# Kernel optimization log

Hardware: AMD Instinct MI355X
Metric: run time of the kernel (lower is better)

Reference implementation:

```python
import jax, jax.numpy as jnp
import numpy as np

N_NODES = 100000
N_EDGES = 1600000
N_PAIRS = 200000
IN_CH = 128
HID_CH = 128


def _graph_conv(x, src, dst, edge_weight, w_rel, b_rel, w_root, num_nodes):
    # PyG GraphConv with aggr='mean':
    # out = lin_rel(mean_{j in N(i)}(x_j * w_ij)) + lin_root(x_i)
    msg = x[src] * edge_weight[:, None]                       # [E, C] gather
    agg = jax.ops.segment_sum(msg, dst, num_segments=num_nodes)  # [N, C]
    cnt = jax.ops.segment_sum(jnp.ones((src.shape[0],), x.dtype), dst,
                              num_segments=num_nodes)          # in-degree
    agg = agg / jnp.maximum(cnt, 1.0)[:, None]                 # mean aggr
    return agg @ w_rel + b_rel + x @ w_root


def setup_inputs() -> dict:
    key = jax.random.key(0)
    ks = jax.random.split(key, 10)
    x = jax.random.normal(ks[0], (N_NODES, IN_CH), dtype=jnp.float32)
    edge_index = jax.random.randint(ks[1], (2, N_EDGES), 0, N_NODES, dtype=jnp.int32)
    edge_weight = jax.random.uniform(ks[2], (N_EDGES,), dtype=jnp.float32)
    edge_label_index = jax.random.randint(ks[3], (2, N_PAIRS), 0, N_NODES, dtype=jnp.int32)
    s1 = 1.0 / np.sqrt(IN_CH)
    s2 = 1.0 / np.sqrt(HID_CH)
    w1_rel = jax.random.uniform(ks[4], (IN_CH, HID_CH), jnp.float32, -s1, s1)
    b1_rel = jnp.zeros((HID_CH,), jnp.float32)
    w1_root = jax.random.uniform(ks[5], (IN_CH, HID_CH), jnp.float32, -s1, s1)
    w2_rel = jax.random.uniform(ks[6], (HID_CH, HID_CH), jnp.float32, -s2, s2)
    b2_rel = jnp.zeros((HID_CH,), jnp.float32)
    w2_root = jax.random.uniform(ks[7], (HID_CH, HID_CH), jnp.float32, -s2, s2)
    return {"x": x, "edge_index": edge_index, "edge_weight": edge_weight,
            "edge_label_index": edge_label_index,
            "w1_rel": w1_rel, "b1_rel": b1_rel, "w1_root": w1_root,
            "w2_rel": w2_rel, "b2_rel": b2_rel, "w2_root": w2_root}


def reference(x, edge_index, edge_weight, edge_label_index,
              w1_rel, b1_rel, w1_root, w2_rel, b2_rel, w2_root):
    src, dst = edge_index[0], edge_index[1]
    # encode
    h = _graph_conv(x, src, dst, edge_weight, w1_rel, b1_rel, w1_root, x.shape[0])
    h = jax.nn.relu(h)
    z = _graph_conv(h, src, dst, edge_weight, w2_rel, b2_rel, w2_root, x.shape[0])
    # decode: scaled dot product between candidate pair embeddings
    zs = z[edge_label_index[0]]   # [P, H]
    zd = z[edge_label_index[1]]   # [P, H]
    scale = z.shape[-1] ** 0.5
    return jnp.sum(zs * zd, axis=-1) / scale
```

## Files before the change

### kernel.cpp

```cpp
#include <hip/hip_runtime.h>

#define NN 100000
#define NE 1600000
#define NP 200000
#define CH 128
#define LK 264

#define BSH 6
#define NB  1563
#define G1  256
#define EPB (NE / G1)
#define CAP3 4096

typedef _Float16 f16x8 __attribute__((ext_vector_type(8)));
typedef _Float16 f16x4 __attribute__((ext_vector_type(4)));
typedef float f32x4 __attribute__((ext_vector_type(4)));

__global__ void cast_kernel(const float* __restrict__ in, _Float16* __restrict__ out, int n8) {
    int i = blockIdx.x * blockDim.x + threadIdx.x;
    if (i >= n8) return;
    const float4* p = (const float4*)in + (size_t)i * 2;
    float4 a = p[0], b = p[1];
    f16x8 o = { (_Float16)a.x, (_Float16)a.y, (_Float16)a.z, (_Float16)a.w,
                (_Float16)b.x, (_Float16)b.y, (_Float16)b.z, (_Float16)b.w };
    *((f16x8*)out + i) = o;
}

__global__ __launch_bounds__(256)
void bucket_hist_kernel(const int* __restrict__ dst, int* __restrict__ hist ) {
    __shared__ int s_h[NB];
    for (int i = threadIdx.x; i < NB; i += 256) s_h[i] = 0;
    __syncthreads();
    int start = blockIdx.x * EPB, end = start + EPB;
    for (int e = start + threadIdx.x; e < end; e += 256)
        atomicAdd(&s_h[dst[e] >> BSH], 1);
    __syncthreads();
    int* row = hist + (size_t)blockIdx.x * NB;
    for (int i = threadIdx.x; i < NB; i += 256) row[i] = s_h[i];
}

__global__ __launch_bounds__(256)
void colscan_kernel(int* __restrict__ hist, int* __restrict__ totals) {
    int b = blockIdx.x * 4 + (threadIdx.x >> 6);
    if (b >= NB) return;
    int lane = threadIdx.x & 63;
    size_t base = (size_t)(lane * 4) * NB + b;
    int v0 = hist[base];
    int v1 = hist[base + NB];
    int v2 = hist[base + 2 * (size_t)NB];
    int v3 = hist[base + 3 * (size_t)NB];
    int s0 = v0, s1 = s0 + v1, s2 = s1 + v2, s3 = s2 + v3;
    int incl = s3;
#pragma unroll
    for (int off = 1; off < 64; off <<= 1) {
        int n = __shfl_up(incl, off, 64);
        if (lane >= off) incl += n;
    }
    int excl = incl - s3;
    hist[base] = excl;
    hist[base + NB] = excl + s0;
    hist[base + 2 * (size_t)NB] = excl + s1;
    hist[base + 3 * (size_t)NB] = excl + s2;
    if (lane == 63) totals[b] = incl;
}

__global__ __launch_bounds__(1024)
void scanB_kernel(const int* __restrict__ totals, int* __restrict__ base) {
    __shared__ int s[2048];
    int tid = threadIdx.x;
    for (int i = tid; i < 2048; i += 1024) s[i] = (i < NB) ? totals[i] : 0;
    __syncthreads();
    for (int off = 1; off < 2048; off <<= 1) {
        int i0 = tid, i1 = tid + 1024;
        int v0 = (i0 >= off) ? s[i0 - off] : 0;
        int v1 = (i1 >= off) ? s[i1 - off] : 0;
        __syncthreads();
        s[i0] += v0; s[i1] += v1;
        __syncthreads();
    }
    if (tid == 0) base[0] = 0;
    for (int i = tid; i < NB; i += 1024) base[i + 1] = s[i];
}

__global__ __launch_bounds__(256)
void bucket_scatter_kernel(const int* __restrict__ src, const int* __restrict__ dst,
                           const float* __restrict__ ew, const int* __restrict__ hist,
                           const int* __restrict__ base, int2* __restrict__ tmp) {
    __shared__ int s_cur[NB];
    const int* row = hist + (size_t)blockIdx.x * NB;
    for (int i = threadIdx.x; i < NB; i += 256) s_cur[i] = base[i] + row[i];
    __syncthreads();
    int start = blockIdx.x * EPB, end = start + EPB;
    for (int e = start + threadIdx.x; e < end; e += 256) {
        int d = dst[e];
        int b = d >> BSH;
        int pos = atomicAdd(&s_cur[b], 1);
        tmp[pos] = make_int2(src[e] | ((d & 63) << 17), __float_as_int(ew[e]));
    }
}

__global__ __launch_bounds__(256)
void bucket_finalize_kernel(const int2* __restrict__ tmp, const int* __restrict__ base,
                            int* __restrict__ row_ptr, int2* __restrict__ csr, int N) {
    __shared__ int2 s_e[CAP3];
    __shared__ int s_cnt[64], s_off[64];
    int b = blockIdx.x;
    int lo = base[b], hi = base[b + 1];
    int size = hi - lo;
    int nbase = b << BSH;
    int ncnt = min(64, N - nbase);
    int tid = threadIdx.x;
    if (tid < 64) s_cnt[tid] = 0;
    bool inlds = (size <= CAP3);
    __syncthreads();
    if (inlds) {
        for (int i = tid; i < size; i += 256) {
            int2 e = tmp[lo + i];
            s_e[i] = e;
            atomicAdd(&s_cnt[(e.x >> 17) & 63], 1);
        }
    } else {
        for (int i = tid; i < size; i += 256) {
            int2 e = tmp[lo + i];
            atomicAdd(&s_cnt[(e.x >> 17) & 63], 1);
        }
    }
    __syncthreads();
    if (tid == 0) {
        int run = 0;
        for (int i = 0; i < 64; i++) { int v = s_cnt[i]; s_off[i] = run; s_cnt[i] = run; run += v; }
    }
    __syncthreads();
    if (tid < ncnt) row_ptr[nbase + tid] = lo + s_off[tid];
    if (b == NB - 1 && tid == 0) row_ptr[N] = hi;
    if (inlds) {
        for (int i = tid; i < size; i += 256) {
            int2 e = s_e[i];
            int dl = (e.x >> 17) & 63;
            int p = atomicAdd(&s_cnt[dl], 1);
            csr[lo + p] = make_int2(e.x & 0x1FFFF, e.y);
        }
    } else {
        for (int i = tid; i < size; i += 256) {
            int2 e = tmp[lo + i];
            int dl = (e.x >> 17) & 63;
            int p = atomicAdd(&s_cnt[dl], 1);
            csr[lo + p] = make_int2(e.x & 0x1FFFF, e.y);
        }
    }
}

__global__ __launch_bounds__(256)
void gather_kernel(const _Float16* __restrict__ feat, const int* __restrict__ row_ptr,
                   const int2* __restrict__ csr, _Float16* __restrict__ agg, int N) {
    int node = blockIdx.x * 4 + (threadIdx.x >> 6);
    if (node >= N) return;
    int lane = threadIdx.x & 63;
    int q = lane >> 4;
    int l16 = lane & 15;
    int c8 = l16 << 3;
    int r0 = row_ptr[node], r1 = row_ptr[node + 1];
    float acc[8] = {0.f, 0.f, 0.f, 0.f, 0.f, 0.f, 0.f, 0.f};
    int r = r0 + q;
    if (r < r1) {
        int2 e = csr[r];
        f16x8 v = *(const f16x8*)&feat[(size_t)e.x * CH + c8];
        for (r += 4; r < r1; r += 4) {
            int2 e2 = csr[r];
            f16x8 v2 = *(const f16x8*)&feat[(size_t)e2.x * CH + c8];
            float w = __int_as_float(e.y);
#pragma unroll
            for (int j = 0; j < 8; j++) acc[j] += w * (float)v[j];
            e = e2; v = v2;
        }
        float w = __int_as_float(e.y);
#pragma unroll
        for (int j = 0; j < 8; j++) acc[j] += w * (float)v[j];
    }
#pragma unroll
    for (int j = 0; j < 8; j++) {
        acc[j] += __shfl_xor(acc[j], 16, 64);
        acc[j] += __shfl_xor(acc[j], 32, 64);
    }
    if (q == 0) {
        float inv = 1.0f / fmaxf((float)(r1 - r0), 1.0f);
        f16x8 o;
#pragma unroll
        for (int j = 0; j < 8; j++) o[j] = (_Float16)(acc[j] * inv);
        *(f16x8*)&agg[(size_t)node * CH + c8] = o;
    }
}

__global__ void prep_w2_kernel(const float* __restrict__ w1r, const float* __restrict__ w1o,
                               const float* __restrict__ w2r, const float* __restrict__ w2o,
                               _Float16* __restrict__ w1t, _Float16* __restrict__ w2t) {
    int idx = blockIdx.x * 256 + threadIdx.x;
    if (idx >= 2 * 128 * 256) return;
    int which = idx >> 15;
    int li = idx & 32767;
    int n = li >> 8, k = li & 255;
    const float* wr = which ? w2r : w1r;
    const float* wo = which ? w2o : w1o;
    _Float16* wt = which ? w2t : w1t;
    float v = (k < 128) ? wr[k * 128 + n] : wo[(k - 128) * 128 + n];
    wt[li] = (_Float16)v;
}

template <bool RELU>
__global__ __launch_bounds__(256)
void layer_mfma_kernel(const _Float16* __restrict__ agg,
                       const _Float16* __restrict__ xin,
                       const _Float16* __restrict__ wt,
                       const float* __restrict__ bias,
                       _Float16* __restrict__ out, int N) {
    __shared__ _Float16 s_a[64][LK];

    const int tid = threadIdx.x;
    const int nb = blockIdx.x * 64;

    for (int i = tid; i < 64 * 32; i += 256) {
        int r = i >> 5;
        int c8 = (i & 31) << 3;
        int gn = nb + r;
        f16x8 v = {};
        if (gn < N) {
            const _Float16* srcp = (c8 < 128) ? &agg[(size_t)gn * CH + c8]
                                              : &xin[(size_t)gn * CH + (c8 - 128)];
            v = *(const f16x8*)srcp;
        }
        *(f16x8*)&s_a[r][c8] = v;
    }
    __syncthreads();

    const int wave = tid >> 6;
    const int lane = tid & 63;
    const int quad = lane >> 4;
    const int l16  = lane & 15;

    f32x4 acc[4][2];
#pragma unroll
    for (int m = 0; m < 4; m++)
#pragma unroll
        for (int t = 0; t < 2; t++) acc[m][t] = (f32x4){0.f, 0.f, 0.f, 0.f};

    const int kq = quad * 8;

#pragma unroll
    for (int ks = 0; ks < 8; ks++) {
        int kbase = ks * 32 + kq;
        f16x8 bf[2];
#pragma unroll
        for (int t = 0; t < 2; t++) {
            int n = wave * 32 + t * 16 + l16;
            bf[t] = *(const f16x8*)&wt[(size_t)n * 256 + kbase];
        }
#pragma unroll
        for (int m = 0; m < 4; m++) {
            f16x8 af = *(const f16x8*)&s_a[m * 16 + l16][kbase];
            acc[m][0] = __builtin_amdgcn_mfma_f32_16x16x32_f16(af, bf[0], acc[m][0], 0, 0, 0);
            acc[m][1] = __builtin_amdgcn_mfma_f32_16x16x32_f16(af, bf[1], acc[m][1], 0, 0, 0);
        }
    }

    float bv[2];
    bv[0] = bias[wave * 32 + l16];
    bv[1] = bias[wave * 32 + 16 + l16];

#pragma unroll
    for (int m = 0; m < 4; m++) {
#pragma unroll
        for (int r = 0; r < 4; r++) {
            int node = nb + m * 16 + quad * 4 + r;
            if (node >= N) continue;
#pragma unroll
            for (int t = 0; t < 2; t++) {
                float v = acc[m][t][r] + bv[t];
                if (RELU) v = fmaxf(v, 0.f);
                out[(size_t)node * CH + wave * 32 + t * 16 + l16] = (_Float16)v;
            }
        }
    }
}

__global__ void decode_kernel(const _Float16* __restrict__ z,
                              const int* __restrict__ ps,
                              const int* __restrict__ pd,
                              float* __restrict__ out, int P) {
    long tid = (long)blockIdx.x * blockDim.x + threadIdx.x;
    int p = (int)(tid >> 5);
    int lane = (int)(tid & 31);
    if (p >= P) return;
    int s = ps[p], d = pd[p];
    f16x4 a = *(const f16x4*)&z[(size_t)s * CH + lane * 4];
    f16x4 b = *(const f16x4*)&z[(size_t)d * CH + lane * 4];
    float v = (float)a[0] * (float)b[0] + (float)a[1] * (float)b[1]
            + (float)a[2] * (float)b[2] + (float)a[3] * (float)b[3];
#pragma unroll
    for (int off = 16; off > 0; off >>= 1) v += __shfl_xor(v, off, 64);
    if (lane == 0) out[p] = v * 0.08838834764831845f;
}

extern "C" void kernel_launch(void* const* d_in, const int* in_sizes, int n_in,
                              void* d_out, int out_size, void* d_ws, size_t ws_size,
                              hipStream_t stream) {
    const float* x       = (const float*)d_in[0];
    const int*   ei      = (const int*)d_in[1];
    const float* ew      = (const float*)d_in[2];
    const int*   eli     = (const int*)d_in[3];
    const float* w1_rel  = (const float*)d_in[4];
    const float* b1      = (const float*)d_in[5];
    const float* w1_root = (const float*)d_in[6];
    const float* w2_rel  = (const float*)d_in[7];
    const float* b2      = (const float*)d_in[8];
    const float* w2_root = (const float*)d_in[9];
    float* out = (float*)d_out;

    const int N = NN, E = NE, P = NP;
    const size_t hrow = (size_t)N * CH * sizeof(_Float16);

    char* ws = (char*)d_ws;
    size_t off = 0;
    auto alloc = [&](size_t bytes) { char* p = ws + off; off = (off + bytes + 15) & ~(size_t)15; return p; };
    _Float16* xh   = (_Float16*)alloc(hrow);
    _Float16* aggh = (_Float16*)alloc(hrow);
    _Float16* hh   = (_Float16*)alloc(hrow);
    _Float16* zh   = aggh;
    int* hist     = (int*)alloc((size_t)G1 * NB * 4);
    int* totals   = (int*)alloc((size_t)NB * 4);
    int* base     = (int*)alloc((size_t)(NB + 1) * 4);
    int* row_ptr  = (int*)alloc((size_t)(N + 1) * 4);
    int2* tmp     = (int2*)alloc((size_t)E * 8);
    int2* csr     = (int2*)alloc((size_t)E * 8);
    _Float16* w1t = (_Float16*)alloc((size_t)128 * 256 * 2);
    _Float16* w2t = (_Float16*)alloc((size_t)128 * 256 * 2);

    const int* src = ei;
    const int* dst = ei + E;

    const int n8 = N * CH / 8;

    cast_kernel<<<(n8 + 255) / 256, 256, 0, stream>>>(x, xh, n8);
    prep_w2_kernel<<<256, 256, 0, stream>>>(w1_rel, w1_root, w2_rel, w2_root, w1t, w2t);

    bucket_hist_kernel<<<G1, 256, 0, stream>>>(dst, hist);
    colscan_kernel<<<(NB + 3) / 4, 256, 0, stream>>>(hist, totals);
    scanB_kernel<<<1, 1024, 0, stream>>>(totals, base);
    bucket_scatter_kernel<<<G1, 256, 0, stream>>>(src, dst, ew, hist, base, tmp);
    bucket_finalize_kernel<<<NB, 256, 0, stream>>>(tmp, base, row_ptr, csr, N);

    gather_kernel<<<(N + 3) / 4, 256, 0, stream>>>(xh, row_ptr, csr, aggh, N);
    layer_mfma_kernel<true><<<(N + 63) / 64, 256, 0, stream>>>(aggh, xh, w1t, b1, hh, N);

    gather_kernel<<<(N + 3) / 4, 256, 0, stream>>>(hh, row_ptr, csr, aggh, N);
    layer_mfma_kernel<false><<<(N + 63) / 64, 256, 0, stream>>>(aggh, hh, w2t, b2, zh, N);

    {
        long threads = (long)P * 32;
        decode_kernel<<<(int)((threads + 255) / 256), 256, 0, stream>>>(zh, eli, eli + P, out, P);
    }
}
```

Before: 387.4 us.

## Fuse prep kernels and accumulate gather in packed fp16 arithmetic

Merges the x-to-fp16 cast, the bucket histogram and the weight transpose into a single launch using block-index ranges, removing two kernel launches. The edge weight is stored as a duplicated fp16 pair in the CSR, and the gather accumulates with packed half2 multiply-adds and half2 shuffles instead of fp32 per-element FMAs. This halves the ALU work and the shuffle count in the gather. The cost is accuracy: summing many neighbours in fp16 adds rounding error and can lose precision for high-degree nodes.

```diff
diff --git a/kernel.cpp b/kernel.cpp
--- a/kernel.cpp
+++ b/kernel.cpp
@@ -11,32 +11,49 @@
 #define G1  256
 #define EPB (NE / G1)
 #define CAP3 4096
+#define NCAST 6250
 
 typedef _Float16 f16x8 __attribute__((ext_vector_type(8)));
 typedef _Float16 f16x4 __attribute__((ext_vector_type(4)));
+typedef _Float16 h2 __attribute__((ext_vector_type(2)));
 typedef float f32x4 __attribute__((ext_vector_type(4)));
 
-__global__ void cast_kernel(const float* __restrict__ in, _Float16* __restrict__ out, int n8) {
-    int i = blockIdx.x * blockDim.x + threadIdx.x;
-    if (i >= n8) return;
-    const float4* p = (const float4*)in + (size_t)i * 2;
-    float4 a = p[0], b = p[1];
-    f16x8 o = { (_Float16)a.x, (_Float16)a.y, (_Float16)a.z, (_Float16)a.w,
-                (_Float16)b.x, (_Float16)b.y, (_Float16)b.z, (_Float16)b.w };
-    *((f16x8*)out + i) = o;
-}
-
-__global__ __launch_bounds__(256)
-void bucket_hist_kernel(const int* __restrict__ dst, int* __restrict__ hist ) {
+__global__ __launch_bounds__(256)
+void fused_prep_kernel(const float* __restrict__ x, _Float16* __restrict__ xh,
+                       const int* __restrict__ dst, int* __restrict__ hist,
+                       const float* __restrict__ w1r, const float* __restrict__ w1o,
+                       const float* __restrict__ w2r, const float* __restrict__ w2o,
+                       _Float16* __restrict__ w1t, _Float16* __restrict__ w2t) {
     __shared__ int s_h[NB];
-    for (int i = threadIdx.x; i < NB; i += 256) s_h[i] = 0;
-    __syncthreads();
-    int start = blockIdx.x * EPB, end = start + EPB;
-    for (int e = start + threadIdx.x; e < end; e += 256)
-        atomicAdd(&s_h[dst[e] >> BSH], 1);
-    __syncthreads();
-    int* row = hist + (size_t)blockIdx.x * NB;
-    for (int i = threadIdx.x; i < NB; i += 256) row[i] = s_h[i];
+    const int bb = blockIdx.x, tid = threadIdx.x;
+    if (bb < NCAST) {
+        int i = bb * 256 + tid;
+        const float4* p = (const float4*)x + (size_t)i * 2;
+        float4 a = p[0], b = p[1];
+        f16x8 o = { (_Float16)a.x, (_Float16)a.y, (_Float16)a.z, (_Float16)a.w,
+                    (_Float16)b.x, (_Float16)b.y, (_Float16)b.z, (_Float16)b.w };
+        *((f16x8*)xh + i) = o;
+    } else if (bb < NCAST + G1) {
+        int g = bb - NCAST;
+        for (int i = tid; i < NB; i += 256) s_h[i] = 0;
+        __syncthreads();
+        int start = g * EPB, end = start + EPB;
+        for (int e = start + tid; e < end; e += 256)
+            atomicAdd(&s_h[dst[e] >> BSH], 1);
+        __syncthreads();
+        int* row = hist + (size_t)g * NB;
+        for (int i = tid; i < NB; i += 256) row[i] = s_h[i];
+    } else {
+        int idx = (bb - NCAST - G1) * 256 + tid;
+        int which = idx >> 15;
+        int li = idx & 32767;
+        int n = li >> 8, k = li & 255;
+        const float* wr = which ? w2r : w1r;
+        const float* wo = which ? w2o : w1o;
+        _Float16* wt = which ? w2t : w1t;
+        float v = (k < 128) ? wr[k * 128 + n] : wo[(k - 128) * 128 + n];
+        wt[li] = (_Float16)v;
+    }
 }
 
 __global__ __launch_bounds__(256)
@@ -95,7 +112,9 @@
         int d = dst[e];
         int b = d >> BSH;
         int pos = atomicAdd(&s_cur[b], 1);
-        tmp[pos] = make_int2(src[e] | ((d & 63) << 17), __float_as_int(ew[e]));
+        _Float16 wh = (_Float16)ew[e];
+        unsigned wy = (unsigned)__builtin_bit_cast(unsigned short, wh) * 0x10001u;
+        tmp[pos] = make_int2(src[e] | ((d & 63) << 17), (int)wy);
     }
 }
 
@@ -160,50 +179,45 @@
     int l16 = lane & 15;
     int c8 = l16 << 3;
     int r0 = row_ptr[node], r1 = row_ptr[node + 1];
-    float acc[8] = {0.f, 0.f, 0.f, 0.f, 0.f, 0.f, 0.f, 0.f};
+    h2 a0 = {}, a1 = {}, a2 = {}, a3 = {};
     int r = r0 + q;
     if (r < r1) {
         int2 e = csr[r];
-        f16x8 v = *(const f16x8*)&feat[(size_t)e.x * CH + c8];
+        uint4 u = *(const uint4*)&feat[(size_t)e.x * CH + c8];
         for (r += 4; r < r1; r += 4) {
             int2 e2 = csr[r];
-            f16x8 v2 = *(const f16x8*)&feat[(size_t)e2.x * CH + c8];
-            float w = __int_as_float(e.y);
-#pragma unroll
-            for (int j = 0; j < 8; j++) acc[j] += w * (float)v[j];
-            e = e2; v = v2;
-        }
-        float w = __int_as_float(e.y);
-#pragma unroll
-        for (int j = 0; j < 8; j++) acc[j] += w * (float)v[j];
-    }
-#pragma unroll
-    for (int j = 0; j < 8; j++) {
-        acc[j] += __shfl_xor(acc[j], 16, 64);
-        acc[j] += __shfl_xor(acc[j], 32, 64);
+            uint4 u2 = *(const uint4*)&feat[(size_t)e2.x * CH + c8];
+            h2 w2 = __builtin_bit_cast(h2, e.y);
+            a0 += w2 * __builtin_bit_cast(h2, u.x);
+            a1 += w2 * __builtin_bit_cast(h2, u.y);
+            a2 += w2 * __builtin_bit_cast(h2, u.z);
+            a3 += w2 * __builtin_bit_cast(h2, u.w);
+            e = e2; u = u2;
+        }
+        h2 w2 = __builtin_bit_cast(h2, e.y);
+        a0 += w2 * __builtin_bit_cast(h2, u.x);
+        a1 += w2 * __builtin_bit_cast(h2, u.y);
+        a2 += w2 * __builtin_bit_cast(h2, u.z);
+        a3 += w2 * __builtin_bit_cast(h2, u.w);
+    }
+#pragma unroll
+    for (int off = 16; off <= 32; off <<= 1) {
+        a0 += __builtin_bit_cast(h2, __shfl_xor(__builtin_bit_cast(int, a0), off, 64));
+        a1 += __builtin_bit_cast(h2, __shfl_xor(__builtin_bit_cast(int, a1), off, 64));
+        a2 += __builtin_bit_cast(h2, __shfl_xor(__builtin_bit_cast(int, a2), off, 64));
+        a3 += __builtin_bit_cast(h2, __shfl_xor(__builtin_bit_cast(int, a3), off, 64));
     }
     if (q == 0) {
         float inv = 1.0f / fmaxf((float)(r1 - r0), 1.0f);
-        f16x8 o;
-#pragma unroll
-        for (int j = 0; j < 8; j++) o[j] = (_Float16)(acc[j] * inv);
-        *(f16x8*)&agg[(size_t)node * CH + c8] = o;
-    }
-}
-
-__global__ void prep_w2_kernel(const float* __restrict__ w1r, const float* __restrict__ w1o,
-                               const float* __restrict__ w2r, const float* __restrict__ w2o,
-                               _Float16* __restrict__ w1t, _Float16* __restrict__ w2t) {
-    int idx = blockIdx.x * 256 + threadIdx.x;
-    if (idx >= 2 * 128 * 256) return;
-    int which = idx >> 15;
-    int li = idx & 32767;
-    int n = li >> 8, k = li & 255;
-    const float* wr = which ? w2r : w1r;
-    const float* wo = which ? w2o : w1o;
-    _Float16* wt = which ? w2t : w1t;
-    float v = (k < 128) ? wr[k * 128 + n] : wo[(k - 128) * 128 + n];
-    wt[li] = (_Float16)v;
+        auto fin = [&](h2 a) -> unsigned {
+            h2 o;
+            o[0] = (_Float16)((float)a[0] * inv);
+            o[1] = (_Float16)((float)a[1] * inv);
+            return __builtin_bit_cast(unsigned, o);
+        };
+        uint4 o = { fin(a0), fin(a1), fin(a2), fin(a3) };
+        *(uint4*)&agg[(size_t)node * CH + c8] = o;
+    }
 }
 
 template <bool RELU>
@@ -337,12 +351,9 @@
     const int* src = ei;
     const int* dst = ei + E;
 
-    const int n8 = N * CH / 8;
-
-    cast_kernel<<<(n8 + 255) / 256, 256, 0, stream>>>(x, xh, n8);
-    prep_w2_kernel<<<256, 256, 0, stream>>>(w1_rel, w1_root, w2_rel, w2_root, w1t, w2t);
-
-    bucket_hist_kernel<<<G1, 256, 0, stream>>>(dst, hist);
+    fused_prep_kernel<<<NCAST + G1 + 256, 256, 0, stream>>>(
+        x, xh, dst, hist, w1_rel, w1_root, w2_rel, w2_root, w1t, w2t);
+
     colscan_kernel<<<(NB + 3) / 4, 256, 0, stream>>>(hist, totals);
     scanB_kernel<<<1, 1024, 0, stream>>>(totals, base);
     bucket_scatter_kernel<<<G1, 256, 0, stream>>>(src, dst, ew, hist, base, tmp);
```

Result: slower. 398.9 us (+3.0%).

## Fuse neighbor gather into MFMA layer kernel and merge prep kernels

Applied to the files above, without the earlier changes.

Each layer's mean-aggregation gather now writes its result straight into the shared-memory A tile of the MFMA GEMM kernel, so the intermediate aggregation buffer is no longer written to and read back from global memory. The cast, histogram and weight-prep kernels are merged into one launch with block-range dispatch, removing two launches. The trade-off is that each 64-node block now does the gather serially, with 16 nodes per wave, before its GEMM. This may lower the memory-level parallelism the standalone gather kernel had across its many small blocks.

```diff
diff --git a/kernel.cpp b/kernel.cpp
--- a/kernel.cpp
+++ b/kernel.cpp
@@ -11,32 +11,48 @@
 #define G1  256
 #define EPB (NE / G1)
 #define CAP3 4096
+#define NCAST 6250
 
 typedef _Float16 f16x8 __attribute__((ext_vector_type(8)));
 typedef _Float16 f16x4 __attribute__((ext_vector_type(4)));
 typedef float f32x4 __attribute__((ext_vector_type(4)));
 
-__global__ void cast_kernel(const float* __restrict__ in, _Float16* __restrict__ out, int n8) {
-    int i = blockIdx.x * blockDim.x + threadIdx.x;
-    if (i >= n8) return;
-    const float4* p = (const float4*)in + (size_t)i * 2;
-    float4 a = p[0], b = p[1];
-    f16x8 o = { (_Float16)a.x, (_Float16)a.y, (_Float16)a.z, (_Float16)a.w,
-                (_Float16)b.x, (_Float16)b.y, (_Float16)b.z, (_Float16)b.w };
-    *((f16x8*)out + i) = o;
-}
-
-__global__ __launch_bounds__(256)
-void bucket_hist_kernel(const int* __restrict__ dst, int* __restrict__ hist ) {
+__global__ __launch_bounds__(256)
+void fused_prep_kernel(const float* __restrict__ x, _Float16* __restrict__ xh,
+                       const int* __restrict__ dst, int* __restrict__ hist,
+                       const float* __restrict__ w1r, const float* __restrict__ w1o,
+                       const float* __restrict__ w2r, const float* __restrict__ w2o,
+                       _Float16* __restrict__ w1t, _Float16* __restrict__ w2t) {
     __shared__ int s_h[NB];
-    for (int i = threadIdx.x; i < NB; i += 256) s_h[i] = 0;
-    __syncthreads();
-    int start = blockIdx.x * EPB, end = start + EPB;
-    for (int e = start + threadIdx.x; e < end; e += 256)
-        atomicAdd(&s_h[dst[e] >> BSH], 1);
-    __syncthreads();
-    int* row = hist + (size_t)blockIdx.x * NB;
-    for (int i = threadIdx.x; i < NB; i += 256) row[i] = s_h[i];
+    const int bb = blockIdx.x, tid = threadIdx.x;
+    if (bb < NCAST) {
+        int i = bb * 256 + tid;
+        const float4* p = (const float4*)x + (size_t)i * 2;
+        float4 a = p[0], b = p[1];
+        f16x8 o = { (_Float16)a.x, (_Float16)a.y, (_Float16)a.z, (_Float16)a.w,
+                    (_Float16)b.x, (_Float16)b.y, (_Float16)b.z, (_Float16)b.w };
+        *((f16x8*)xh + i) = o;
+    } else if (bb < NCAST + G1) {
+        int g = bb - NCAST;
+        for (int i = tid; i < NB; i += 256) s_h[i] = 0;
+        __syncthreads();
+        int start = g * EPB, end = start + EPB;
+        for (int e = start + tid; e < end; e += 256)
+            atomicAdd(&s_h[dst[e] >> BSH], 1);
+        __syncthreads();
+        int* row = hist + (size_t)g * NB;
+        for (int i = tid; i < NB; i += 256) row[i] = s_h[i];
+    } else {
+        int idx = (bb - NCAST - G1) * 256 + tid;
+        int which = idx >> 15;
+        int li = idx & 32767;
+        int n = li >> 8, k = li & 255;
+        const float* wr = which ? w2r : w1r;
+        const float* wo = which ? w2o : w1o;
+        _Float16* wt = which ? w2t : w1t;
+        float v = (k < 128) ? wr[k * 128 + n] : wo[(k - 128) * 128 + n];
+        wt[li] = (_Float16)v;
+    }
 }
 
 __global__ __launch_bounds__(256)
@@ -150,101 +166,75 @@
     }
 }
 
-__global__ __launch_bounds__(256)
-void gather_kernel(const _Float16* __restrict__ feat, const int* __restrict__ row_ptr,
-                   const int2* __restrict__ csr, _Float16* __restrict__ agg, int N) {
-    int node = blockIdx.x * 4 + (threadIdx.x >> 6);
-    if (node >= N) return;
-    int lane = threadIdx.x & 63;
-    int q = lane >> 4;
-    int l16 = lane & 15;
-    int c8 = l16 << 3;
-    int r0 = row_ptr[node], r1 = row_ptr[node + 1];
-    float acc[8] = {0.f, 0.f, 0.f, 0.f, 0.f, 0.f, 0.f, 0.f};
-    int r = r0 + q;
-    if (r < r1) {
-        int2 e = csr[r];
-        f16x8 v = *(const f16x8*)&feat[(size_t)e.x * CH + c8];
-        for (r += 4; r < r1; r += 4) {
-            int2 e2 = csr[r];
-            f16x8 v2 = *(const f16x8*)&feat[(size_t)e2.x * CH + c8];
-            float w = __int_as_float(e.y);
-#pragma unroll
-            for (int j = 0; j < 8; j++) acc[j] += w * (float)v[j];
-            e = e2; v = v2;
-        }
-        float w = __int_as_float(e.y);
-#pragma unroll
-        for (int j = 0; j < 8; j++) acc[j] += w * (float)v[j];
-    }
-#pragma unroll
-    for (int j = 0; j < 8; j++) {
-        acc[j] += __shfl_xor(acc[j], 16, 64);
-        acc[j] += __shfl_xor(acc[j], 32, 64);
-    }
-    if (q == 0) {
-        float inv = 1.0f / fmaxf((float)(r1 - r0), 1.0f);
-        f16x8 o;
-#pragma unroll
-        for (int j = 0; j < 8; j++) o[j] = (_Float16)(acc[j] * inv);
-        *(f16x8*)&agg[(size_t)node * CH + c8] = o;
-    }
-}
-
-__global__ void prep_w2_kernel(const float* __restrict__ w1r, const float* __restrict__ w1o,
-                               const float* __restrict__ w2r, const float* __restrict__ w2o,
-                               _Float16* __restrict__ w1t, _Float16* __restrict__ w2t) {
-    int idx = blockIdx.x * 256 + threadIdx.x;
-    if (idx >= 2 * 128 * 256) return;
-    int which = idx >> 15;
-    int li = idx & 32767;
-    int n = li >> 8, k = li & 255;
-    const float* wr = which ? w2r : w1r;
-    const float* wo = which ? w2o : w1o;
-    _Float16* wt = which ? w2t : w1t;
-    float v = (k < 128) ? wr[k * 128 + n] : wo[(k - 128) * 128 + n];
-    wt[li] = (_Float16)v;
-}
-
 template <bool RELU>
 __global__ __launch_bounds__(256)
-void layer_mfma_kernel(const _Float16* __restrict__ agg,
-                       const _Float16* __restrict__ xin,
-                       const _Float16* __restrict__ wt,
-                       const float* __restrict__ bias,
-                       _Float16* __restrict__ out, int N) {
-    __shared__ _Float16 s_a[64][LK];
+void gatherlayer_kernel(const _Float16* __restrict__ feat, const int* __restrict__ row_ptr,
+                        const int2* __restrict__ csr, const _Float16* __restrict__ wt,
+                        const float* __restrict__ bias, _Float16* __restrict__ out, int N) {
+    __shared__ _Float16 atile[64][LK];
 
     const int tid = threadIdx.x;
-    const int nb = blockIdx.x * 64;
-
-    for (int i = tid; i < 64 * 32; i += 256) {
-        int r = i >> 5;
-        int c8 = (i & 31) << 3;
-        int gn = nb + r;
-        f16x8 v = {};
-        if (gn < N) {
-            const _Float16* srcp = (c8 < 128) ? &agg[(size_t)gn * CH + c8]
-                                              : &xin[(size_t)gn * CH + (c8 - 128)];
-            v = *(const f16x8*)srcp;
-        }
-        *(f16x8*)&s_a[r][c8] = v;
-    }
-    __syncthreads();
-
+    const int nb = blockIdx.x << BSH;
     const int wave = tid >> 6;
     const int lane = tid & 63;
+    const int q = lane >> 4;
+    const int l16 = lane & 15;
+    const int c8 = l16 << 3;
+
+    for (int nn = 0; nn < 16; nn++) {
+        int local_n = wave * 16 + nn;
+        int node = nb + local_n;
+        if (node >= N) break;
+        int r0 = row_ptr[node], r1 = row_ptr[node + 1];
+        float acc[8] = {0.f, 0.f, 0.f, 0.f, 0.f, 0.f, 0.f, 0.f};
+        int r = r0 + q;
+        if (r < r1) {
+            int2 e = csr[r];
+            f16x8 v = *(const f16x8*)&feat[(size_t)e.x * CH + c8];
+            for (r += 4; r < r1; r += 4) {
+                int2 e2 = csr[r];
+                f16x8 v2 = *(const f16x8*)&feat[(size_t)e2.x * CH + c8];
+                float w = __int_as_float(e.y);
+#pragma unroll
+                for (int j = 0; j < 8; j++) acc[j] += w * (float)v[j];
+                e = e2; v = v2;
+            }
+            float w = __int_as_float(e.y);
+#pragma unroll
+            for (int j = 0; j < 8; j++) acc[j] += w * (float)v[j];
+        }
+#pragma unroll
+        for (int j = 0; j < 8; j++) {
+            acc[j] += __shfl_xor(acc[j], 16, 64);
+            acc[j] += __shfl_xor(acc[j], 32, 64);
+        }
+        if (q == 0) {
+            float inv = 1.0f / fmaxf((float)(r1 - r0), 1.0f);
+            f16x8 o;
+#pragma unroll
+            for (int j = 0; j < 8; j++) o[j] = (_Float16)(acc[j] * inv);
+            *(f16x8*)&atile[local_n][c8] = o;
+        }
+    }
+
+    for (int i = tid; i < 64 * 16; i += 256) {
+        int rrow = i >> 4;
+        int cc8 = (i & 15) << 3;
+        int gn = nb + rrow;
+        f16x8 v = {};
+        if (gn < N) v = *(const f16x8*)&feat[(size_t)gn * CH + cc8];
+        *(f16x8*)&atile[rrow][128 + cc8] = v;
+    }
+    __syncthreads();
+
     const int quad = lane >> 4;
-    const int l16  = lane & 15;
-
-    f32x4 acc[4][2];
+    f32x4 ac[4][2];
 #pragma unroll
     for (int m = 0; m < 4; m++)
 #pragma unroll
-        for (int t = 0; t < 2; t++) acc[m][t] = (f32x4){0.f, 0.f, 0.f, 0.f};
+        for (int t = 0; t < 2; t++) ac[m][t] = (f32x4){0.f, 0.f, 0.f, 0.f};
 
     const int kq = quad * 8;
-
 #pragma unroll
     for (int ks = 0; ks < 8; ks++) {
         int kbase = ks * 32 + kq;
@@ -256,9 +246,9 @@
         }
 #pragma unroll
         for (int m = 0; m < 4; m++) {
-            f16x8 af = *(const f16x8*)&s_a[m * 16 + l16][kbase];
-            acc[m][0] = __builtin_amdgcn_mfma_f32_16x16x32_f16(af, bf[0], acc[m][0], 0, 0, 0);
-            acc[m][1] = __builtin_amdgcn_mfma_f32_16x16x32_f16(af, bf[1], acc[m][1], 0, 0, 0);
+            f16x8 af = *(const f16x8*)&atile[m * 16 + l16][kbase];
+            ac[m][0] = __builtin_amdgcn_mfma_f32_16x16x32_f16(af, bf[0], ac[m][0], 0, 0, 0);
+            ac[m][1] = __builtin_amdgcn_mfma_f32_16x16x32_f16(af, bf[1], ac[m][1], 0, 0, 0);
         }
     }
 
@@ -274,7 +264,7 @@
             if (node >= N) continue;
 #pragma unroll
             for (int t = 0; t < 2; t++) {
-                float v = acc[m][t][r] + bv[t];
+                float v = ac[m][t][r] + bv[t];
                 if (RELU) v = fmaxf(v, 0.f);
                 out[(size_t)node * CH + wave * 32 + t * 16 + l16] = (_Float16)v;
             }
@@ -321,10 +311,9 @@
     char* ws = (char*)d_ws;
     size_t off = 0;
     auto alloc = [&](size_t bytes) { char* p = ws + off; off = (off + bytes + 15) & ~(size_t)15; return p; };
-    _Float16* xh   = (_Float16*)alloc(hrow);
-    _Float16* aggh = (_Float16*)alloc(hrow);
-    _Float16* hh   = (_Float16*)alloc(hrow);
-    _Float16* zh   = aggh;
+    _Float16* xh  = (_Float16*)alloc(hrow);
+    _Float16* hh  = (_Float16*)alloc(hrow);
+    _Float16* zh  = (_Float16*)alloc(hrow);
     int* hist     = (int*)alloc((size_t)G1 * NB * 4);
     int* totals   = (int*)alloc((size_t)NB * 4);
     int* base     = (int*)alloc((size_t)(NB + 1) * 4);
@@ -337,22 +326,16 @@
     const int* src = ei;
     const int* dst = ei + E;
 
-    const int n8 = N * CH / 8;
-
-    cast_kernel<<<(n8 + 255) / 256, 256, 0, stream>>>(x, xh, n8);
-    prep_w2_kernel<<<256, 256, 0, stream>>>(w1_rel, w1_root, w2_rel, w2_root, w1t, w2t);
-
-    bucket_hist_kernel<<<G1, 256, 0, stream>>>(dst, hist);
+    fused_prep_kernel<<<NCAST + G1 + 256, 256, 0, stream>>>(
+        x, xh, dst, hist, w1_rel, w1_root, w2_rel, w2_root, w1t, w2t);
+
     colscan_kernel<<<(NB + 3) / 4, 256, 0, stream>>>(hist, totals);
     scanB_kernel<<<1, 1024, 0, stream>>>(totals, base);
     bucket_scatter_kernel<<<G1, 256, 0, stream>>>(src, dst, ew, hist, base, tmp);
     bucket_finalize_kernel<<<NB, 256, 0, stream>>>(tmp, base, row_ptr, csr, N);
 
-    gather_kernel<<<(N + 3) / 4, 256, 0, stream>>>(xh, row_ptr, csr, aggh, N);
-    layer_mfma_kernel<true><<<(N + 63) / 64, 256, 0, stream>>>(aggh, xh, w1t, b1, hh, N);
-
-    gather_kernel<<<(N + 3) / 4, 256, 0, stream>>>(hh, row_ptr, csr, aggh, N);
-    layer_mfma_kernel<false><<<(N + 63) / 64, 256, 0, stream>>>(aggh, hh, w2t, b2, zh, N);
+    gatherlayer_kernel<true><<<NB, 256, 0, stream>>>(xh, row_ptr, csr, w1t, b1, hh, N);
+    gatherlayer_kernel<false><<<NB, 256, 0, stream>>>(hh, row_ptr, csr, w2t, b2, zh, N);
 
     {
         long threads = (long)P * 32;
```

Result: slower. 425.0 us (+9.7%).
